# Optimization experiments

Measured on AMD Instinct MI355X. Metric: run time of the kernel, lower is better.

## Reference

```python
import jax, jax.numpy as jnp
import numpy as np
import math

B, T, C, H = 4, 2048, 1024, 16
HS = C // H
EPS = 1e-5


def layernorm(x, g, b):
    mu = jnp.mean(x, axis=-1, keepdims=True)
    var = jnp.var(x, axis=-1, keepdims=True)
    return (x - mu) * jax.lax.rsqrt(var + EPS) * g + b


def setup_inputs() -> dict:
    key = jax.random.key(0)
    ks = jax.random.split(key, 7)
    rn = lambda k, s: jax.random.normal(k, s, dtype=jnp.float32) * 0.02
    return {
        "x": jax.random.normal(ks[0], (B, T, C), dtype=jnp.float32),
        "mask": jnp.tril(jnp.ones((T, T), dtype=jnp.int32)),  # causal tril buffer
        "wq": rn(ks[1], (H, HS, C)),  # stacked per-head Linear weights [out,in]
        "wk": rn(ks[2], (H, HS, C)),
        "wv": rn(ks[3], (H, HS, C)),
        "ln1_g": jnp.ones((C,), jnp.float32),
        "ln1_b": jnp.zeros((C,), jnp.float32),
        "ln2_g": jnp.ones((C,), jnp.float32),
        "ln2_b": jnp.zeros((C,), jnp.float32),
        "w1": rn(ks[4], (4 * C, C)),
        "b1": jnp.zeros((4 * C,), jnp.float32),
        "w2": rn(ks[5], (C, 4 * C)),
        "b2": jnp.zeros((C,), jnp.float32),
    }


def reference(x, mask, wq, wk, wv, ln1_g, ln1_b, ln2_g, ln2_b, w1, b1, w2, b2):
    Bx, Tx, Cx = x.shape
    h = layernorm(x, ln1_g, ln1_b)
    # per-head projections, batched over heads: [B,H,T,HS]
    q = jnp.einsum('btc,hdc->bhtd', h, wq)
    k = jnp.einsum('btc,hdc->bhtd', h, wk)
    v = jnp.einsum('btc,hdc->bhtd', h, wv)
    scores = jnp.einsum('bhtd,bhsd->bhts', q, k) * (1.0 / math.sqrt(HS))
    scores = jnp.where(mask[None, None, :Tx, :Tx] == 0, -jnp.inf, scores)
    w = jax.nn.softmax(scores, axis=-1)
    attn = jnp.einsum('bhts,bhsd->bhtd', w, v)  # [B,H,T,HS]
    attn = attn.transpose(0, 2, 1, 3).reshape(Bx, Tx, Cx)  # concat heads
    x = x + attn
    h2 = layernorm(x, ln2_g, ln2_b)
    ff = jax.nn.silu(h2 @ w1.T + b1) @ w2.T + b2  # dropout = identity (eval)
    return x + ff
```

## Files before the change

kernel.cpp:

```cpp
#include <hip/hip_runtime.h>
#include <stdint.h>

#define Bb 4
#define Tt 2048
#define Cc 1024
#define Hh 16
#define HSs 64

typedef __attribute__((ext_vector_type(8))) __bf16 bf16x8;
typedef __attribute__((ext_vector_type(4))) float f32x4;

__device__ __forceinline__ ushort f2bf(float f){
  union { float f; uint u; } c; c.f = f;
  return (ushort)((c.u + 0x8000u) >> 16);
}
__device__ __forceinline__ float bf2f(ushort u){
  union { uint u; float f; } c; c.u = ((uint)u) << 16; return c.f;
}

__device__ __forceinline__ void gload16(const void* g, void* l){
  __builtin_amdgcn_global_load_lds(
      (__attribute__((address_space(1))) void*)(g),
      (__attribute__((address_space(3))) void*)(l), 16, 0, 0);
}

__global__ __launch_bounds__(256) void cast_all_kernel(
    const float* __restrict__ wq, const float* __restrict__ wk,
    const float* __restrict__ wv, const float* __restrict__ w1,
    const float* __restrict__ w2, ushort* __restrict__ out){
  int i = (blockIdx.x * 256 + threadIdx.x) * 4;
  const float* src; int off;
  if      (i <  1048576){ src = wq; off = i; }
  else if (i <  2097152){ src = wk; off = i - 1048576; }
  else if (i <  3145728){ src = wv; off = i - 2097152; }
  else if (i <  7340032){ src = w1; off = i - 3145728; }
  else                  { src = w2; off = i - 7340032; }
  float4 v = *(const float4*)(src + off);
  ushort4 o; o.x = f2bf(v.x); o.y = f2bf(v.y); o.z = f2bf(v.z); o.w = f2bf(v.w);
  *(ushort4*)(out + i) = o;
}

__global__ __launch_bounds__(256) void add_p1_kernel(float* __restrict__ out,
                                                     const ushort* __restrict__ p1b){
  for (int it = 0; it < 4; ++it){
    size_t i = ((size_t)it * 2048 * 256 + blockIdx.x * 256 + threadIdx.x) * 4;
    float4 o = *(const float4*)(out + i);
    ushort4 p = *(const ushort4*)(p1b + i);
    o.x += bf2f(p.x); o.y += bf2f(p.y); o.z += bf2f(p.z); o.w += bf2f(p.w);
    *(float4*)(out + i) = o;
  }
}

__global__ __launch_bounds__(256) void ln1_kernel(const float* __restrict__ x,
    const float* __restrict__ gw, const float* __restrict__ bw,
    ushort* __restrict__ hout){
  int row = blockIdx.x, tid = threadIdx.x;
  size_t base = (size_t)row * Cc + tid * 4;
  float4 xv = *(const float4*)(x + base);
  float s  = xv.x + xv.y + xv.z + xv.w;
  float ss = xv.x*xv.x + xv.y*xv.y + xv.z*xv.z + xv.w*xv.w;
  #pragma unroll
  for (int off = 1; off < 64; off <<= 1){ s += __shfl_xor(s, off); ss += __shfl_xor(ss, off); }
  __shared__ float red[8];
  int wid = tid >> 6, lane = tid & 63;
  if (lane == 0){ red[wid] = s; red[4 + wid] = ss; }
  __syncthreads();
  s  = red[0] + red[1] + red[2] + red[3];
  ss = red[4] + red[5] + red[6] + red[7];
  float mu = s * (1.0f / Cc);
  float rstd = rsqrtf(ss * (1.0f / Cc) - mu * mu + 1e-5f);
  float4 gv = *(const float4*)(gw + tid * 4);
  float4 bv = *(const float4*)(bw + tid * 4);
  ushort4 o;
  o.x = f2bf((xv.x - mu) * rstd * gv.x + bv.x);
  o.y = f2bf((xv.y - mu) * rstd * gv.y + bv.y);
  o.z = f2bf((xv.z - mu) * rstd * gv.z + bv.z);
  o.w = f2bf((xv.w - mu) * rstd * gv.w + bv.w);
  *(ushort4*)(hout + base) = o;
}

__global__ __launch_bounds__(256) void ln2_kernel(const float* __restrict__ x,
    const ushort* __restrict__ attnb,
    const float* __restrict__ gw, const float* __restrict__ bw,
    float* __restrict__ x2, ushort* __restrict__ hout){
  int row = blockIdx.x, tid = threadIdx.x;
  size_t base = (size_t)row * Cc + tid * 4;
  float4 xv = *(const float4*)(x + base);
  ushort4 av = *(const ushort4*)(attnb + base);
  xv.x += bf2f(av.x); xv.y += bf2f(av.y); xv.z += bf2f(av.z); xv.w += bf2f(av.w);
  *(float4*)(x2 + base) = xv;
  float s  = xv.x + xv.y + xv.z + xv.w;
  float ss = xv.x*xv.x + xv.y*xv.y + xv.z*xv.z + xv.w*xv.w;
  #pragma unroll
  for (int off = 1; off < 64; off <<= 1){ s += __shfl_xor(s, off); ss += __shfl_xor(ss, off); }
  __shared__ float red[8];
  int wid = tid >> 6, lane = tid & 63;
  if (lane == 0){ red[wid] = s; red[4 + wid] = ss; }
  __syncthreads();
  s  = red[0] + red[1] + red[2] + red[3];
  ss = red[4] + red[5] + red[6] + red[7];
  float mu = s * (1.0f / Cc);
  float rstd = rsqrtf(ss * (1.0f / Cc) - mu * mu + 1e-5f);
  float4 gv = *(const float4*)(gw + tid * 4);
  float4 bv = *(const float4*)(bw + tid * 4);
  ushort4 o;
  o.x = f2bf((xv.x - mu) * rstd * gv.x + bv.x);
  o.y = f2bf((xv.y - mu) * rstd * gv.y + bv.y);
  o.z = f2bf((xv.z - mu) * rstd * gv.z + bv.z);
  o.w = f2bf((xv.w - mu) * rstd * gv.w + bv.w);
  *(ushort4*)(hout + base) = o;
}

#define MFMA_QUAD(AF, SI, QI, BQ) \
  { \
    _Pragma("unroll") \
    for (int mi = 0; mi < 4; ++mi){ \
      acc[(SI)*4+mi][(QI)*2+0] = __builtin_amdgcn_mfma_f32_16x16x32_bf16(AF[mi][0], BQ[0][0], acc[(SI)*4+mi][(QI)*2+0], 0,0,0); \
      acc[(SI)*4+mi][(QI)*2+0] = __builtin_amdgcn_mfma_f32_16x16x32_bf16(AF[mi][1], BQ[0][1], acc[(SI)*4+mi][(QI)*2+0], 0,0,0); \
      acc[(SI)*4+mi][(QI)*2+1] = __builtin_amdgcn_mfma_f32_16x16x32_bf16(AF[mi][0], BQ[1][0], acc[(SI)*4+mi][(QI)*2+1], 0,0,0); \
      acc[(SI)*4+mi][(QI)*2+1] = __builtin_amdgcn_mfma_f32_16x16x32_bf16(AF[mi][1], BQ[1][1], acc[(SI)*4+mi][(QI)*2+1], 0,0,0); \
    } \
  }

#define GEMM_TOP() { asm volatile("s_waitcnt lgkmcnt(0)" ::: "memory"); \
                     __builtin_amdgcn_sched_barrier(0); __builtin_amdgcn_s_setprio(1); }
#define GEMM_MID() { __builtin_amdgcn_s_setprio(0); }
#define GEMM_BAR() { __builtin_amdgcn_s_barrier(); }

template<int MODE>
__device__ __forceinline__ void gemm256_body(
    const ushort* __restrict__ A, const ushort* __restrict__ Bw,
    int N, int K, int ldO,
    ushort* __restrict__ obf, float* __restrict__ of32,
    ushort* __restrict__ p1b, const float* __restrict__ bias)
{
  __shared__ __align__(16) ushort lds[2][2][2][128 * 64];
  int tid = threadIdx.x, lane = tid & 63, wid = tid >> 6;
  int wm = wid >> 2, wn = wid & 3;
  int c = lane & 15, g = lane >> 4;
  int brow0 = (wn & 1) * 64;

  int nwg = gridDim.x, bid = blockIdx.x;
  int wgid = (bid & 7) * (nwg >> 3) + (bid >> 3);
  int m0, n0, koff = 0;
  if (MODE == 3){
    int split = wgid >> 7, rem = wgid & 127;
    m0 = (rem >> 2) << 8; n0 = (rem & 3) << 8; koff = split << 11;
  } else {
    int nTn = N >> 8;
    m0 = (wgid / nTn) << 8; n0 = (wgid % nTn) << 8;
  }

  const ushort* Ag = A  + (size_t)m0 * K + koff;
  const ushort* Bg = Bw + (size_t)n0 * K + koff;

  auto stage = [&](const ushort* gbase, int t, int ab, int hb){
    #pragma unroll
    for (int j = 0; j < 2; ++j){
      int d = j * 8192 + wid * 1024 + lane * 16;
      int row = d >> 7;
      int colb = (d & 127) ^ ((row & 7) << 4);
      gload16((const char*)gbase + ((size_t)(hb * 128 + row) * K + t * 64) * 2 + colb,
              (char*)&lds[t & 1][ab][hb][0] + j * 8192 + wid * 1024);
    }
  };

  f32x4 acc[8][4] = {};
  bf16x8 af0[4][2], af1[4][2], bq0[2][2], bq1[2][2];

  auto readA = [&](const char* Ap, int sub, bf16x8 (&af)[4][2]){
    #pragma unroll
    for (int mi = 0; mi < 4; ++mi){
      int row = sub * 64 + mi * 16 + c, sw = (row & 7) << 4;
      af[mi][0] = *(const bf16x8*)(Ap + row * 128 + ((g * 16) ^ sw));
      af[mi][1] = *(const bf16x8*)(Ap + row * 128 + ((64 + g * 16) ^ sw));
    }
  };
  auto readB = [&](const char* Bp, int hb, bf16x8 (&bq)[2][2]){
    #pragma unroll
    for (int nj = 0; nj < 2; ++nj){
      int row = brow0 + hb * 32 + nj * 16 + c, sw = (row & 7) << 4;
      bq[nj][0] = *(const bf16x8*)(Bp + row * 128 + ((g * 16) ^ sw));
      bq[nj][1] = *(const bf16x8*)(Bp + row * 128 + ((64 + g * 16) ^ sw));
    }
  };

  int nt = (MODE == 3) ? (K >> 7) : (K >> 6);

  stage(Ag, 0, 0, 0); stage(Ag, 0, 0, 1);
  stage(Bg, 0, 1, 0); stage(Bg, 0, 1, 1);
  if (nt > 1){
    stage(Bg, 1, 1, 0); stage(Bg, 1, 1, 1);
    stage(Ag, 1, 0, 0); stage(Ag, 1, 0, 1);
    asm volatile("s_waitcnt vmcnt(8)" ::: "memory");
  } else {
    asm volatile("s_waitcnt vmcnt(0)" ::: "memory");
  }
  __builtin_amdgcn_s_barrier();
  readA((const char*)&lds[0][0][wm][0], 0, af0);
  readB((const char*)&lds[0][1][wn >> 1][0], 0, bq0);

  for (int t = 0; t < nt; ++t){
    const char* Abuf  = (const char*)&lds[t & 1][0][wm][0];
    const char* Bbuf  = (const char*)&lds[t & 1][1][wn >> 1][0];
    const char* AbufN = (const char*)&lds[(t + 1) & 1][0][wm][0];
    const char* BbufN = (const char*)&lds[(t + 1) & 1][1][wn >> 1][0];

    GEMM_TOP();
    MFMA_QUAD(af0, 0, 0, bq0);
    GEMM_MID();
    readB(Bbuf, 1, bq1);
    GEMM_BAR();

    GEMM_TOP();
    MFMA_QUAD(af0, 0, 1, bq1);
    GEMM_MID();
    readA(Abuf, 1, af1);
    GEMM_BAR();

    GEMM_TOP();
    MFMA_QUAD(af1, 1, 0, bq0);
    GEMM_MID();
    if (t + 2 < nt){
      stage(Bg, t + 2, 1, 0);
      asm volatile("s_waitcnt vmcnt(2)" ::: "memory");
    } else {
      asm volatile("s_waitcnt vmcnt(0)" ::: "memory");
    }
    GEMM_BAR();

    GEMM_TOP();
    MFMA_QUAD(af1, 1, 1, bq1);
    GEMM_MID();
    if (t + 1 < nt){
      readA(AbufN, 0, af0);
      readB(BbufN, 0, bq0);
    }
    if (t + 2 < nt){
      stage(Bg, t + 2, 1, 1);
      stage(Ag, t + 2, 0, 0);
      stage(Ag, t + 2, 0, 1);
    }
    GEMM_BAR();
  }

  #pragma unroll
  for (int mi = 0; mi < 8; ++mi){
    #pragma unroll
    for (int ni = 0; ni < 4; ++ni){
      #pragma unroll
      for (int r = 0; r < 4; ++r){
        float v = acc[mi][ni][r];
        int m = m0 + wm * 128 + mi * 16 + g * 4 + r;
        int n = n0 + wn * 64 + ni * 16 + c;
        if (MODE == 0){
          int which = n >> 10;
          int nn = n & 1023;
          int b = m >> 11, t = m & (Tt - 1);
          int h = nn >> 6, d = nn & 63;
          float vv = (which == 0) ? v * 0.125f : v;
          size_t base = (size_t)which * (size_t)(Bb * Tt * Cc);
          size_t idx = (which == 2)
              ? ((((size_t)(b * Hh + h)) * HSs + d) * Tt + t)
              : ((((size_t)(b * Hh + h)) * Tt + t) * HSs + d);
          obf[base + idx] = f2bf(vv);
        } else if (MODE == 1){
          v += bias[n];
          float sv = v / (1.0f + __expf(-v));
          obf[(size_t)m * ldO + n] = f2bf(sv);
        } else {
          size_t idx = (size_t)m * N + n;
          if (koff == 0) of32[idx] = of32[idx] + v + bias[n];
          else           p1b[idx] = f2bf(v);
        }
      }
    }
  }
}

__global__ __launch_bounds__(512, 2) void gemm_qkv_kernel(
    const ushort* __restrict__ A, const ushort* __restrict__ Bw, int N, int K,
    ushort* __restrict__ obf){
  gemm256_body<0>(A, Bw, N, K, 0, obf, nullptr, nullptr, nullptr);
}
__global__ __launch_bounds__(512, 2) void gemm_ffn1_kernel(
    const ushort* __restrict__ A, const ushort* __restrict__ Bw, int N, int K, int ldO,
    ushort* __restrict__ obf, const float* __restrict__ bias){
  gemm256_body<1>(A, Bw, N, K, ldO, obf, nullptr, nullptr, bias);
}
__global__ __launch_bounds__(512, 2) void gemm_ffn2_kernel(
    const ushort* __restrict__ A, const ushort* __restrict__ Bw, int N, int K,
    float* __restrict__ of32, ushort* __restrict__ p1b, const float* __restrict__ bias){
  gemm256_body<3>(A, Bw, N, K, N, nullptr, of32, p1b, bias);
}

__global__ __launch_bounds__(256, 2) void attn_kernel(
    const ushort* __restrict__ q, const ushort* __restrict__ k,
    const ushort* __restrict__ vt, ushort* __restrict__ attnb)
{
  __shared__ __align__(16) ushort Ksm[4][64 * 64];
  __shared__ __align__(16) ushort Vsm[4][64 * 64];
  __shared__ __align__(16) ushort Pl[4][32 * 64];

  int bh  = blockIdx.y;
  int p   = blockIdx.x;
  int tid = threadIdx.x, wid = tid >> 6, lane = tid & 63;
  int g = lane >> 4, c = lane & 15;
  int qbA = 15 - p, qbB = p;
  int q0A = qbA * 128 + wid * 32;
  int q0B = qbB * 128 + wid * 32;
  const ushort* Qb = q  + (size_t)bh * Tt * HSs;
  const ushort* Kb = k  + (size_t)bh * Tt * HSs;
  const ushort* Vt = vt + (size_t)bh * HSs * Tt;
  char* Pw = (char*)&Pl[wid][0];

  auto stageKV = [&](int bsel, int s0){
    #pragma unroll
    for (int hb = 0; hb < 2; ++hb){
      int i = wid + hb * 4;
      int row = i * 8 + (lane >> 3);
      int col = ((lane & 7) ^ (row & 7)) * 8;
      gload16(Kb + (size_t)(s0 + row) * HSs + col, &Ksm[bsel][i * 512]);
      gload16(Vt + (size_t)row * Tt + s0 + col,    &Vsm[bsel][i * 512]);
    }
  };

  bf16x8 qfA[2][2], qfB[2][2];
  #pragma unroll
  for (int mi = 0; mi < 2; ++mi)
    #pragma unroll
    for (int ks = 0; ks < 2; ++ks){
      qfA[mi][ks] = *(const bf16x8*)(Qb + (size_t)(q0A + mi * 16 + c) * HSs + ks * 32 + g * 8);
      qfB[mi][ks] = *(const bf16x8*)(Qb + (size_t)(q0B + mi * 16 + c) * HSs + ks * 32 + g * 8);
    }

  f32x4 oA[2][4] = {}, oB[2][4] = {};
  float mA[2][4], lA[2][4], mB[2][4], lB[2][4];
  #pragma unroll
  for (int mi = 0; mi < 2; ++mi)
    #pragma unroll
    for (int r = 0; r < 4; ++r){
      mA[mi][r] = -1e30f; lA[mi][r] = 0.f;
      mB[mi][r] = -1e30f; lB[mi][r] = 0.f;
    }

  auto computeTile = [&](bf16x8 (&qf)[2][2], f32x4 (&o)[2][4],
                         float (&mrow)[2][4], float (&lpart)[2][4],
                         int q0w, int s0, const char* Kbuf, const char* Vbuf){
    f32x4 S[2][4] = {};
    bf16x8 kf[4][2];
    #pragma unroll
    for (int ni = 0; ni < 4; ++ni)
      #pragma unroll
      for (int ks = 0; ks < 2; ++ks)
        kf[ni][ks] = *(const bf16x8*)(Kbuf + (ni * 16 + c) * 128 + (((ks * 4 + g) ^ (c & 7)) << 4));
    #pragma unroll
    for (int mi = 0; mi < 2; ++mi)
      #pragma unroll
      for (int ni = 0; ni < 4; ++ni)
        #pragma unroll
        for (int ks = 0; ks < 2; ++ks)
          S[mi][ni] = __builtin_amdgcn_mfma_f32_16x16x32_bf16(qf[mi][ks], kf[ni][ks], S[mi][ni], 0, 0, 0);

    if (s0 + 63 > q0w){
      #pragma unroll
      for (int mi = 0; mi < 2; ++mi)
        #pragma unroll
        for (int ni = 0; ni < 4; ++ni)
          #pragma unroll
          for (int r = 0; r < 4; ++r){
            int tl = q0w + mi * 16 + g * 4 + r, sl = s0 + ni * 16 + c;
            if (sl > tl) S[mi][ni][r] = -1e30f;
          }
    }

    float lmax[2][4], worst = -1e30f;
    #pragma unroll
    for (int mi = 0; mi < 2; ++mi)
      #pragma unroll
      for (int r = 0; r < 4; ++r){
        float a0 = fmaxf(S[mi][0][r], S[mi][1][r]);
        float a1 = fmaxf(S[mi][2][r], S[mi][3][r]);
        lmax[mi][r] = fmaxf(a0, a1);
        worst = fmaxf(worst, lmax[mi][r] - mrow[mi][r]);
      }
    if (!__all(worst <= 8.0f)){
      #pragma unroll
      for (int mi = 0; mi < 2; ++mi)
        #pragma unroll
        for (int r = 0; r < 4; ++r){
          float mx = lmax[mi][r];
          mx = fmaxf(mx, __shfl_xor(mx, 1));
          mx = fmaxf(mx, __shfl_xor(mx, 2));
          mx = fmaxf(mx, __shfl_xor(mx, 4));
          mx = fmaxf(mx, __shfl_xor(mx, 8));
          float mnew  = fmaxf(mrow[mi][r], mx);
          float alpha = __expf(mrow[mi][r] - mnew);
          lpart[mi][r] *= alpha;
          #pragma unroll
          for (int dt = 0; dt < 4; ++dt) o[mi][dt][r] *= alpha;
          mrow[mi][r] = mnew;
        }
    }
    #pragma unroll
    for (int mi = 0; mi < 2; ++mi)
      #pragma unroll
      for (int r = 0; r < 4; ++r){
        int row = mi * 16 + g * 4 + r;
        float mb = mrow[mi][r] * 1.44269504f;
        float pp[4];
        #pragma unroll
        for (int ni = 0; ni < 4; ++ni){
          pp[ni] = exp2f(__builtin_fmaf(S[mi][ni][r], 1.44269504f, -mb));
          *(ushort*)(Pw + row * 128 + (((ni * 32 + 2 * c) ^ ((row & 7) << 4)))) = f2bf(pp[ni]);
        }
        lpart[mi][r] += (pp[0] + pp[1]) + (pp[2] + pp[3]);
      }

    bf16x8 vf[4][2];
    #pragma unroll
    for (int dt = 0; dt < 4; ++dt)
      #pragma unroll
      for (int ks = 0; ks < 2; ++ks)
        vf[dt][ks] = *(const bf16x8*)(Vbuf + (dt * 16 + c) * 128 + (((ks * 4 + g) ^ (c & 7)) << 4));
    #pragma unroll
    for (int mi = 0; mi < 2; ++mi){
      #pragma unroll
      for (int ks = 0; ks < 2; ++ks){
        bf16x8 pf = *(const bf16x8*)(Pw + (mi * 16 + c) * 128 + ((((ks * 4 + g) ^ (c & 7)) << 4)));
        #pragma unroll
        for (int dt = 0; dt < 4; ++dt)
          o[mi][dt] = __builtin_amdgcn_mfma_f32_16x16x32_bf16(pf, vf[dt][ks], o[mi][dt], 0, 0, 0);
      }
    }
  };

  int nchA = 2 * qbA + 2;

  stageKV(0, 0);
  stageKV(1, 64);

  for (int ch = 0; ch < nchA; ch += 2){
    bool staged = (ch + 2 < nchA);
    if (staged){
      stageKV((ch + 2) & 3, (ch + 2) * 64);
      stageKV((ch + 3) & 3, (ch + 3) * 64);
      asm volatile("s_waitcnt vmcnt(8)" ::: "memory");
    } else {
      asm volatile("s_waitcnt vmcnt(0)" ::: "memory");
    }
    __builtin_amdgcn_sched_barrier(0);
    __builtin_amdgcn_s_barrier();

    {
      int s0 = ch * 64;
      const char* Kbuf = (const char*)&Ksm[ch & 3][0];
      const char* Vbuf = (const char*)&Vsm[ch & 3][0];
      if (s0 <= q0A + 31) computeTile(qfA, oA, mA, lA, q0A, s0, Kbuf, Vbuf);
      if (s0 <= q0B + 31) computeTile(qfB, oB, mB, lB, q0B, s0, Kbuf, Vbuf);
    }
    {
      int s0 = (ch + 1) * 64;
      const char* Kbuf = (const char*)&Ksm[(ch + 1) & 3][0];
      const char* Vbuf = (const char*)&Vsm[(ch + 1) & 3][0];
      if (s0 <= q0A + 31) computeTile(qfA, oA, mA, lA, q0A, s0, Kbuf, Vbuf);
      if (s0 <= q0B + 31) computeTile(qfB, oB, mB, lB, q0B, s0, Kbuf, Vbuf);
    }

    __builtin_amdgcn_sched_barrier(0);
    __builtin_amdgcn_s_barrier();
  }

  int b = bh >> 4, h = bh & 15;
  #pragma unroll
  for (int mi = 0; mi < 2; ++mi)
    #pragma unroll
    for (int r = 0; r < 4; ++r){
      float la = lA[mi][r];
      la += __shfl_xor(la, 1); la += __shfl_xor(la, 2);
      la += __shfl_xor(la, 4); la += __shfl_xor(la, 8);
      float lia = 1.0f / la;
      float lb = lB[mi][r];
      lb += __shfl_xor(lb, 1); lb += __shfl_xor(lb, 2);
      lb += __shfl_xor(lb, 4); lb += __shfl_xor(lb, 8);
      float lib = 1.0f / lb;
      #pragma unroll
      for (int dt = 0; dt < 4; ++dt){
        int tA = q0A + mi * 16 + g * 4 + r;
        int tB = q0B + mi * 16 + g * 4 + r;
        attnb[((size_t)(b * Tt + tA)) * Cc + h * HSs + dt * 16 + c] = f2bf(oA[mi][dt][r] * lia);
        attnb[((size_t)(b * Tt + tB)) * Cc + h * HSs + dt * 16 + c] = f2bf(oB[mi][dt][r] * lib);
      }
    }
}

extern "C" void kernel_launch(void* const* d_in, const int* in_sizes, int n_in,
                              void* d_out, int out_size, void* d_ws, size_t ws_size,
                              hipStream_t stream) {
  (void)in_sizes; (void)n_in; (void)out_size; (void)ws_size;
  const float* x    = (const float*)d_in[0];
  const float* wq   = (const float*)d_in[2];
  const float* wk   = (const float*)d_in[3];
  const float* wv   = (const float*)d_in[4];
  const float* ln1g = (const float*)d_in[5];
  const float* ln1b = (const float*)d_in[6];
  const float* ln2g = (const float*)d_in[7];
  const float* ln2b = (const float*)d_in[8];
  const float* w1   = (const float*)d_in[9];
  const float* b1   = (const float*)d_in[10];
  const float* w2   = (const float*)d_in[11];
  const float* b2   = (const float*)d_in[12];
  float* out = (float*)d_out;

  char* ws = (char*)d_ws;
  const size_t SZ_ACT = (size_t)Bb * Tt * Cc * 2;
  ushort* h1    = (ushort*)(ws);
  ushort* qbuf  = (ushort*)(ws + SZ_ACT);
  ushort* kbuf  = (ushort*)(ws + 2 * SZ_ACT);
  ushort* vbuf  = (ushort*)(ws + 3 * SZ_ACT);
  ushort* attnb = (ushort*)(ws + 4 * SZ_ACT);
  ushort* h2    = (ushort*)(ws + 5 * SZ_ACT);
  ushort* h3    = (ushort*)(ws + 6 * SZ_ACT);
  ushort* p1b   = (ushort*)(ws + SZ_ACT);
  char*   wsw   = ws + 6 * SZ_ACT + (size_t)Bb * Tt * 4 * Cc * 2;
  ushort* wqb = (ushort*)(wsw);
  ushort* w1b = (ushort*)(wsw + 3 * (size_t)Cc * Cc * 2);
  ushort* w2b = (ushort*)(wsw + 3 * (size_t)Cc * Cc * 2 + (size_t)4 * Cc * Cc * 2);

  cast_all_kernel<<<dim3(11264), 256, 0, stream>>>(wq, wk, wv, w1, w2, wqb);

  ln1_kernel<<<dim3(Bb * Tt), 256, 0, stream>>>(x, ln1g, ln1b, h1);

  gemm_qkv_kernel<<<dim3(32 * 12), 512, 0, stream>>>(h1, wqb, 3 * Cc, Cc, qbuf);

  attn_kernel<<<dim3(8, Bb * Hh), 256, 0, stream>>>(qbuf, kbuf, vbuf, attnb);

  ln2_kernel<<<dim3(Bb * Tt), 256, 0, stream>>>(x, attnb, ln2g, ln2b, out, h2);

  gemm_ffn1_kernel<<<dim3(32 * 8), 512, 0, stream>>>(h2, w1b,                      2048, Cc, 4 * Cc, h3,        b1);
  gemm_ffn1_kernel<<<dim3(32 * 8), 512, 0, stream>>>(h2, w1b + (size_t)2048 * Cc,  2048, Cc, 4 * Cc, h3 + 2048, b1 + 2048);
  gemm_ffn2_kernel<<<dim3(256), 512, 0, stream>>>(h3, w2b, Cc, 4 * Cc, out, p1b, b2);
  add_p1_kernel<<<dim3(2048), 256, 0, stream>>>(out, p1b);
}
```

Baseline: 395.1 us.

## Switch attention to double-buffered KV with 3 blocks/CU; split FFN2 partial sums to bf16

The attention kernel drops from a 4-deep KV ring staged two chunks at a time to a 2-buffer, one-chunk-ahead pipeline. This halves K/V shared memory so launch bounds can request 3 blocks per CU. Separately, the FFN2 split-K no longer does a read-modify-write of the fp32 output in the first half. Both halves now write bf16 partials, and the final add kernel sums both partials plus the bias. The costs are less prefetch depth in attention, an extra bf16 rounding of the first partial, and one more partial buffer to read.

```diff
diff --git a/kernel.cpp b/kernel.cpp
--- a/kernel.cpp
+++ b/kernel.cpp
@@ -40,13 +40,20 @@
   *(ushort4*)(out + i) = o;
 }
 
-__global__ __launch_bounds__(256) void add_p1_kernel(float* __restrict__ out,
-                                                     const ushort* __restrict__ p1b){
+__global__ __launch_bounds__(256) void add_pp_kernel(float* __restrict__ out,
+    const ushort* __restrict__ p0b, const ushort* __restrict__ p1b,
+    const float* __restrict__ bias){
   for (int it = 0; it < 4; ++it){
-    size_t i = ((size_t)it * 2048 * 256 + blockIdx.x * 256 + threadIdx.x) * 4;
+    size_t i4 = (size_t)it * 2048 * 256 + blockIdx.x * 256 + threadIdx.x;
+    size_t i = i4 * 4;
     float4 o = *(const float4*)(out + i);
-    ushort4 p = *(const ushort4*)(p1b + i);
-    o.x += bf2f(p.x); o.y += bf2f(p.y); o.z += bf2f(p.z); o.w += bf2f(p.w);
+    ushort4 a = *(const ushort4*)(p0b + i);
+    ushort4 b = *(const ushort4*)(p1b + i);
+    float4 bv = *(const float4*)(bias + ((i4 & 255) * 4));
+    o.x += bf2f(a.x) + bf2f(b.x) + bv.x;
+    o.y += bf2f(a.y) + bf2f(b.y) + bv.y;
+    o.z += bf2f(a.z) + bf2f(b.z) + bv.z;
+    o.w += bf2f(a.w) + bf2f(b.w) + bv.w;
     *(float4*)(out + i) = o;
   }
 }
@@ -270,7 +277,7 @@
           obf[(size_t)m * ldO + n] = f2bf(sv);
         } else {
           size_t idx = (size_t)m * N + n;
-          if (koff == 0) of32[idx] = of32[idx] + v + bias[n];
+          if (koff == 0) obf[idx] = f2bf(v);
           else           p1b[idx] = f2bf(v);
         }
       }
@@ -290,16 +297,16 @@
 }
 __global__ __launch_bounds__(512, 2) void gemm_ffn2_kernel(
     const ushort* __restrict__ A, const ushort* __restrict__ Bw, int N, int K,
-    float* __restrict__ of32, ushort* __restrict__ p1b, const float* __restrict__ bias){
-  gemm256_body<3>(A, Bw, N, K, N, nullptr, of32, p1b, bias);
-}
-
-__global__ __launch_bounds__(256, 2) void attn_kernel(
+    ushort* __restrict__ p0b, ushort* __restrict__ p1b){
+  gemm256_body<3>(A, Bw, N, K, N, p0b, nullptr, p1b, nullptr);
+}
+
+__global__ __launch_bounds__(256, 3) void attn_kernel(
     const ushort* __restrict__ q, const ushort* __restrict__ k,
     const ushort* __restrict__ vt, ushort* __restrict__ attnb)
 {
-  __shared__ __align__(16) ushort Ksm[4][64 * 64];
-  __shared__ __align__(16) ushort Vsm[4][64 * 64];
+  __shared__ __align__(16) ushort Ksm[2][64 * 64];
+  __shared__ __align__(16) ushort Vsm[2][64 * 64];
   __shared__ __align__(16) ushort Pl[4][32 * 64];
 
   int bh  = blockIdx.y;
@@ -438,35 +445,20 @@
   int nchA = 2 * qbA + 2;
 
   stageKV(0, 0);
-  stageKV(1, 64);
-
-  for (int ch = 0; ch < nchA; ch += 2){
-    bool staged = (ch + 2 < nchA);
-    if (staged){
-      stageKV((ch + 2) & 3, (ch + 2) * 64);
-      stageKV((ch + 3) & 3, (ch + 3) * 64);
-      asm volatile("s_waitcnt vmcnt(8)" ::: "memory");
-    } else {
-      asm volatile("s_waitcnt vmcnt(0)" ::: "memory");
-    }
-    __builtin_amdgcn_sched_barrier(0);
-    __builtin_amdgcn_s_barrier();
-
-    {
-      int s0 = ch * 64;
-      const char* Kbuf = (const char*)&Ksm[ch & 3][0];
-      const char* Vbuf = (const char*)&Vsm[ch & 3][0];
-      if (s0 <= q0A + 31) computeTile(qfA, oA, mA, lA, q0A, s0, Kbuf, Vbuf);
-      if (s0 <= q0B + 31) computeTile(qfB, oB, mB, lB, q0B, s0, Kbuf, Vbuf);
-    }
-    {
-      int s0 = (ch + 1) * 64;
-      const char* Kbuf = (const char*)&Ksm[(ch + 1) & 3][0];
-      const char* Vbuf = (const char*)&Vsm[(ch + 1) & 3][0];
-      if (s0 <= q0A + 31) computeTile(qfA, oA, mA, lA, q0A, s0, Kbuf, Vbuf);
-      if (s0 <= q0B + 31) computeTile(qfB, oB, mB, lB, q0B, s0, Kbuf, Vbuf);
-    }
-
+  asm volatile("s_waitcnt vmcnt(0)" ::: "memory");
+  __builtin_amdgcn_s_barrier();
+
+  for (int ch = 0; ch < nchA; ++ch){
+    int buf = ch & 1;
+    if (ch + 1 < nchA) stageKV(buf ^ 1, (ch + 1) * 64);
+
+    int s0 = ch * 64;
+    const char* Kbuf = (const char*)&Ksm[buf][0];
+    const char* Vbuf = (const char*)&Vsm[buf][0];
+    if (s0 <= q0A + 31) computeTile(qfA, oA, mA, lA, q0A, s0, Kbuf, Vbuf);
+    if (s0 <= q0B + 31) computeTile(qfB, oB, mB, lB, q0B, s0, Kbuf, Vbuf);
+
+    asm volatile("s_waitcnt vmcnt(0) lgkmcnt(0)" ::: "memory");
     __builtin_amdgcn_sched_barrier(0);
     __builtin_amdgcn_s_barrier();
   }
@@ -521,7 +513,8 @@
   ushort* attnb = (ushort*)(ws + 4 * SZ_ACT);
   ushort* h2    = (ushort*)(ws + 5 * SZ_ACT);
   ushort* h3    = (ushort*)(ws + 6 * SZ_ACT);
-  ushort* p1b   = (ushort*)(ws + SZ_ACT);
+  ushort* p0b   = (ushort*)(ws + SZ_ACT);
+  ushort* p1b   = (ushort*)(ws + 2 * SZ_ACT);
   char*   wsw   = ws + 6 * SZ_ACT + (size_t)Bb * Tt * 4 * Cc * 2;
   ushort* wqb = (ushort*)(wsw);
   ushort* w1b = (ushort*)(wsw + 3 * (size_t)Cc * Cc * 2);
@@ -539,6 +532,6 @@
 
   gemm_ffn1_kernel<<<dim3(32 * 8), 512, 0, stream>>>(h2, w1b,                      2048, Cc, 4 * Cc, h3,        b1);
   gemm_ffn1_kernel<<<dim3(32 * 8), 512, 0, stream>>>(h2, w1b + (size_t)2048 * Cc,  2048, Cc, 4 * Cc, h3 + 2048, b1 + 2048);
-  gemm_ffn2_kernel<<<dim3(256), 512, 0, stream>>>(h3, w2b, Cc, 4 * Cc, out, p1b, b2);
-  add_p1_kernel<<<dim3(2048), 256, 0, stream>>>(out, p1b);
-}
+  gemm_ffn2_kernel<<<dim3(256), 512, 0, stream>>>(h3, w2b, Cc, 4 * Cc, p0b, p1b);
+  add_pp_kernel<<<dim3(2048), 256, 0, stream>>>(out, p0b, p1b, b2);
+}
```

After: 587.2 us. 48.6% more time.
